# Kernel optimization log

Hardware: AMD Instinct MI355X
Metric: run time of the kernel (lower is better)

## Reference

```python
import jax, jax.numpy as jnp
import numpy as np
import math

SLIDING_WINDOW = 1024  # matches init kwarg

def setup_inputs() -> dict:
    key = jax.random.key(0)
    ks = jax.random.split(key, 6)
    B, S, Hq, Hkv, D = 1, 2048, 32, 8, 128
    NUM_PAGES, STRIDE = 300, 16
    q = jax.random.normal(ks[0], (B, S, Hq, D), dtype=jnp.float32)
    k = jax.random.normal(ks[1], (B, S, Hkv, D), dtype=jnp.float32)
    v = jax.random.normal(ks[2], (B, S, Hkv, D), dtype=jnp.float32)
    sink = jax.random.normal(ks[3], (Hq,), dtype=jnp.float32)
    cache_state = jnp.zeros((NUM_PAGES, STRIDE, 2, Hkv, D), dtype=jnp.float32)
    seq_block_ids = jax.random.randint(ks[4], (B, S // STRIDE), 0, NUM_PAGES, dtype=jnp.int64)
    return {"q": q, "k": k, "v": v, "sink": sink,
            "cache_state": cache_state, "seq_block_ids": seq_block_ids}


def reference(q, k, v, sink, cache_state, seq_block_ids):
    B, S, Hq, D = q.shape
    Hkv = k.shape[2]
    stride = cache_state.shape[1]

    # --- paged cache write (prefill side effect) ---
    kv = jnp.stack([k, v], axis=2)                       # [B,S,2,Hkv,D]
    pages = kv.reshape(B * (S // stride), stride, 2, Hkv, D)
    _ = cache_state.at[seq_block_ids.reshape(-1)].set(pages)

    # --- decomposed attention: matmul + mask + softmax(+sink) + matmul ---
    rep = Hq // Hkv
    ke = jnp.repeat(k, rep, axis=2)                      # [B,S,Hq,D] (GQA expand)
    ve = jnp.repeat(v, rep, axis=2)
    scale = 1.0 / math.sqrt(D)
    scores = jnp.einsum('bihd,bjhd->bhij', q, ke) * scale  # [B,Hq,S,S]

    i = jnp.arange(S)[:, None]
    j = jnp.arange(S)[None, :]
    allowed = (j <= i) & (i - j < SLIDING_WINDOW)        # causal + sliding window
    neg = jnp.finfo(scores.dtype).min
    logits = jnp.where(allowed, scores, neg)

    # attention sink: extra per-head logit appended; contributes to denominator only
    sink_l = jnp.broadcast_to(sink[None, :, None, None], (B, Hq, S, 1))
    probs = jax.nn.softmax(jnp.concatenate([logits, sink_l], axis=-1), axis=-1)[..., :S]

    out = jnp.einsum('bhij,bjhd->bihd', probs, ve)       # [B,S,Hq,D]
    return out
```

## Files before the change

kernel.cpp:

```cpp
#include <hip/hip_runtime.h>
#include <hip/hip_bf16.h>


#define S_LEN 2048
#define DH    128
#define HQ    32
#define HKV   8
#define WIN   1024
#define BR    64
#define BC    32
#define NT    (S_LEN / BC)
#define FM    16.0f
#define TILE_CH 512

typedef unsigned short u16;
typedef __attribute__((ext_vector_type(8))) short  short8;
typedef __attribute__((ext_vector_type(4))) float  floatx4;
typedef __attribute__((ext_vector_type(4))) unsigned int uintx4;

__device__ __forceinline__ unsigned rne1(float a) {
    unsigned u = __float_as_uint(a);
    return (u + 0x7FFFu + ((u >> 16) & 1u)) >> 16;
}
__device__ __forceinline__ unsigned rne_pk(float a, float b) {
    return rne1(a) | (rne1(b) << 16);
}

__global__ __launch_bounds__(256) void pack_kv(const float* __restrict__ kg,
                                               const float* __restrict__ vg,
                                               u16* __restrict__ kp,
                                               u16* __restrict__ vtp)
{
    __shared__ float Vs[BC][DH + 1];
    const int b   = blockIdx.x;
    const int hk  = b >> 6;
    const int jt  = b & 63;
    const int tid = threadIdx.x;
    const int j0  = jt * BC;

    #pragma unroll
    for (int t = 0; t < 4; t++) {
        int idx = tid + t * 256;
        int j   = idx >> 5;
        int dc  = idx & 31;
        floatx4 f = *(const floatx4*)(vg + ((size_t)(j0 + j) * HKV + hk) * DH + dc * 4);
        Vs[j][dc * 4 + 0] = f[0]; Vs[j][dc * 4 + 1] = f[1];
        Vs[j][dc * 4 + 2] = f[2]; Vs[j][dc * 4 + 3] = f[3];
    }

    u16* kpt = kp + (size_t)b * TILE_CH * 8;
    #pragma unroll
    for (int t = 0; t < 2; t++) {
        int c = tid + t * 256;
        int row = c >> 4, cc = c & 15;
        const float* p = kg + ((size_t)(j0 + row) * HKV + hk) * DH + cc * 8;
        floatx4 f0 = *(const floatx4*)p;
        floatx4 f1 = *(const floatx4*)(p + 4);
        int pc = (row << 4) | (cc ^ (row & 7));
        *(uintx4*)(kpt + pc * 8) =
            (uintx4){rne_pk(f0[0], f0[1]), rne_pk(f0[2], f0[3]),
                     rne_pk(f1[0], f1[1]), rne_pk(f1[2], f1[3])};
    }
    __syncthreads();

    u16* vpt = vtp + (size_t)b * TILE_CH * 8;
    #pragma unroll
    for (int t = 0; t < 2; t++) {
        int q  = tid + t * 256;
        int dd = q >> 2, c = q & 3;
        unsigned w0 = rne_pk(Vs[c * 4 + 0][dd], Vs[c * 4 + 16][dd]);
        unsigned w1 = rne_pk(Vs[c * 4 + 1][dd], Vs[c * 4 + 17][dd]);
        unsigned w2 = rne_pk(Vs[c * 4 + 2][dd], Vs[c * 4 + 18][dd]);
        unsigned w3 = rne_pk(Vs[c * 4 + 3][dd], Vs[c * 4 + 19][dd]);
        int qp = (dd << 2) | (c ^ ((dd >> 2) & 3));
        *(uintx4*)(vpt + qp * 8) = (uintx4){w0, w1, w2, w3};
    }
}

__launch_bounds__(256, 4)
__global__ void fa_kernel(const float* __restrict__ qg,
                          const u16* __restrict__ kp,
                          const u16* __restrict__ vtp,
                          const float* __restrict__ sg,
                          float* __restrict__ outg)
{
    __shared__ __align__(16) u16 Kt[2][TILE_CH * 8];
    __shared__ __align__(16) u16 Vt[2][TILE_CH * 8];
    __shared__ __align__(16) u16 Pb[BR * 40];

    const int tid  = threadIdx.x;
    const int w    = tid >> 6;
    const int lane = tid & 63;
    const int quad = lane >> 4;
    const int l16  = lane & 15;

    const int qb = blockIdx.x / HQ;
    const int h  = blockIdx.x % HQ;
    const int hk = h >> 2;
    const int i0 = qb * BR;
    const int m0 = i0 + w * 16;

    short8 qf[4];
    {
        const float* qrow = qg + ((size_t)(m0 + l16) * HQ + h) * DH;
        #pragma unroll
        for (int kk = 0; kk < 4; kk++) {
            const float* p = qrow + kk * 32 + quad * 8;
            floatx4 f0 = *(const floatx4*)p;
            floatx4 f1 = *(const floatx4*)(p + 4);
            uintx4 u = (uintx4){rne_pk(f0[0], f0[1]), rne_pk(f0[2], f0[3]),
                                rne_pk(f1[0], f1[1]), rne_pk(f1[2], f1[3])};
            qf[kk] = *(short8*)&u;
        }
    }

    floatx4 acc[8];
    #pragma unroll
    for (int i = 0; i < 8; i++) acc[i] = (floatx4){0.f, 0.f, 0.f, 0.f};
    float l_part[4] = {0.f, 0.f, 0.f, 0.f};

    int c_r[4];
    #pragma unroll
    for (int r = 0; r < 4; r++) c_r[r] = m0 + quad * 4 + r - l16;

    int jlo = i0 - (WIN - 1); if (jlo < 0) jlo = 0;
    const int jt_lo = jlo >> 5;
    const int jt_hi = (i0 + BR - 1) >> 5;

    const float SC2 = 0.08838834764831845f * 1.4426950408889634f;

    const int ch0 = w * 64 + lane;
    auto stage = [&](int bb, int jt) {
        const u16* kpt = kp  + ((size_t)(hk * NT + jt)) * TILE_CH * 8;
        const u16* vpt = vtp + ((size_t)(hk * NT + jt)) * TILE_CH * 8;
        #pragma unroll
        for (int it = 0; it < 2; it++) {
            int ch = ch0 + it * 256;
            __builtin_amdgcn_global_load_lds(
                (const __attribute__((address_space(1))) unsigned*)(kpt + ch * 8),
                (__attribute__((address_space(3))) unsigned*)(&Kt[bb][ch * 8]), 16, 0, 0);
            __builtin_amdgcn_global_load_lds(
                (const __attribute__((address_space(1))) unsigned*)(vpt + ch * 8),
                (__attribute__((address_space(3))) unsigned*)(&Vt[bb][ch * 8]), 16, 0, 0);
        }
    };

    stage(0, jt_lo);
    int bb = 0;

    for (int jt = jt_lo; jt <= jt_hi; jt++) {
        const int j0 = jt << 5;

        __syncthreads();

        if (jt < jt_hi) stage(bb ^ 1, jt + 1);

        floatx4 sc[2];
        sc[0] = (floatx4){0.f, 0.f, 0.f, 0.f};
        sc[1] = (floatx4){0.f, 0.f, 0.f, 0.f};
        #pragma unroll
        for (int kk = 0; kk < 4; kk++) {
            #pragma unroll
            for (int n = 0; n < 2; n++) {
                int row = n * 16 + l16;
                int cc  = kk * 4 + quad;
                int pc  = (row << 4) | (cc ^ (row & 7));
                short8 kf = *(const short8*)(&Kt[bb][pc * 8]);
                sc[n] = __builtin_amdgcn_mfma_f32_16x16x32_bf16(qf[kk], kf, sc[n], 0, 0, 0);
            }
        }

        const int prow0 = w * 16 + quad * 4;
        const bool interior = (j0 + (BC - 1) <= i0) && (j0 >= i0 + BR - WIN);
        if (interior) {
            #pragma unroll
            for (int r = 0; r < 4; r++) {
                float p0 = exp2f(fmaf(sc[0][r], SC2, -FM));
                float p1 = exp2f(fmaf(sc[1][r], SC2, -FM));
                l_part[r] += p0 + p1;
                *(unsigned*)(&Pb[(prow0 + r) * 40 + l16 * 2]) = rne_pk(p0, p1);
            }
        } else {
            #pragma unroll
            for (int r = 0; r < 4; r++) {
                bool a0 = (j0 <= c_r[r]) && (j0 > c_r[r] - WIN);
                bool a1 = (j0 + 16 <= c_r[r]) && (j0 + 16 > c_r[r] - WIN);
                float p0 = a0 ? exp2f(fmaf(sc[0][r], SC2, -FM)) : 0.f;
                float p1 = a1 ? exp2f(fmaf(sc[1][r], SC2, -FM)) : 0.f;
                l_part[r] += p0 + p1;
                *(unsigned*)(&Pb[(prow0 + r) * 40 + l16 * 2]) = rne_pk(p0, p1);
            }
        }

        {
            short8 pf = *(const short8*)(&Pb[(w * 16 + l16) * 40 + quad * 8]);
            #pragma unroll
            for (int nf = 0; nf < 8; nf++) {
                int dd = nf * 16 + l16;
                int qp = (dd << 2) | (quad ^ ((dd >> 2) & 3));
                short8 vf = *(const short8*)(&Vt[bb][qp * 8]);
                acc[nf] = __builtin_amdgcn_mfma_f32_16x16x32_bf16(pf, vf, acc[nf], 0, 0, 0);
            }
        }
        bb ^= 1;
    }

    const float sk2 = exp2f(fmaf(sg[h], 1.4426950408889634f, -FM));
    float inv[4];
    #pragma unroll
    for (int r = 0; r < 4; r++) {
        float l = l_part[r];
        #pragma unroll
        for (int off = 1; off < 16; off <<= 1)
            l += __shfl_xor(l, off);
        inv[r] = 1.f / (l + sk2);
    }
    #pragma unroll
    for (int nf = 0; nf < 8; nf++) {
        int d = nf * 16 + l16;
        #pragma unroll
        for (int r = 0; r < 4; r++) {
            int ig = m0 + quad * 4 + r;
            outg[((size_t)ig * HQ + h) * DH + d] = acc[nf][r] * inv[r];
        }
    }
}

__launch_bounds__(256, 4)
__global__ void fa_fallback(const float* __restrict__ qg,
                            const float* __restrict__ kg,
                            const float* __restrict__ vg,
                            const float* __restrict__ sg,
                            float* __restrict__ outg)
{
    __shared__ __align__(16) u16 Kt[BC * DH];
    __shared__ __align__(16) u16 Vt[DH * BC];
    __shared__ __align__(16) u16 Pb[BR * 40];

    const int tid  = threadIdx.x;
    const int w    = tid >> 6;
    const int lane = tid & 63;
    const int quad = lane >> 4;
    const int l16  = lane & 15;

    const int qb = blockIdx.x / HQ;
    const int h  = blockIdx.x % HQ;
    const int hk = h >> 2;
    const int i0 = qb * BR;
    const int m0 = i0 + w * 16;

    short8 qf[4];
    {
        const float* qrow = qg + ((size_t)(m0 + l16) * HQ + h) * DH;
        #pragma unroll
        for (int kk = 0; kk < 4; kk++) {
            const float* p = qrow + kk * 32 + quad * 8;
            floatx4 f0 = *(const floatx4*)p;
            floatx4 f1 = *(const floatx4*)(p + 4);
            uintx4 u = (uintx4){rne_pk(f0[0], f0[1]), rne_pk(f0[2], f0[3]),
                                rne_pk(f1[0], f1[1]), rne_pk(f1[2], f1[3])};
            qf[kk] = *(short8*)&u;
        }
    }

    floatx4 acc[8];
    #pragma unroll
    for (int i = 0; i < 8; i++) acc[i] = (floatx4){0.f, 0.f, 0.f, 0.f};
    float l_part[4] = {0.f, 0.f, 0.f, 0.f};

    int jlo = i0 - (WIN - 1); if (jlo < 0) jlo = 0;
    const int jt_lo = jlo >> 5;
    const int jt_hi = (i0 + BR - 1) >> 5;
    const float SC2 = 0.08838834764831845f * 1.4426950408889634f;

    for (int jt = jt_lo; jt <= jt_hi; jt++) {
        const int j0 = jt << 5;
        __syncthreads();
        #pragma unroll
        for (int it = 0; it < 2; it++) {
            int g   = tid + 256 * it;
            int row = g >> 4, cc = g & 15;
            int pc  = (row << 4) | (cc ^ (row & 7));
            const float* kpp = kg + ((size_t)(j0 + row) * HKV + hk) * DH + cc * 8;
            floatx4 f0 = *(const floatx4*)kpp;
            floatx4 f1 = *(const floatx4*)(kpp + 4);
            *(uintx4*)(&Kt[pc * 8]) =
                (uintx4){rne_pk(f0[0], f0[1]), rne_pk(f0[2], f0[3]),
                         rne_pk(f1[0], f1[1]), rne_pk(f1[2], f1[3])};
        }
        #pragma unroll
        for (int it = 0; it < 2; it++) {
            int g  = tid + 256 * it;
            int d  = g & 127, jc = g >> 7;
            const float* vp = vg + ((size_t)(j0 + jc * 8) * HKV + hk) * DH + d;
            float e0 = vp[0 * HKV * DH], e1 = vp[1 * HKV * DH];
            float e2 = vp[2 * HKV * DH], e3 = vp[3 * HKV * DH];
            float e4 = vp[4 * HKV * DH], e5 = vp[5 * HKV * DH];
            float e6 = vp[6 * HKV * DH], e7 = vp[7 * HKV * DH];
            int pc = (d << 2) | (jc ^ ((d >> 2) & 3));
            *(uintx4*)(&Vt[pc * 8]) =
                (uintx4){rne_pk(e0, e1), rne_pk(e2, e3), rne_pk(e4, e5), rne_pk(e6, e7)};
        }
        __syncthreads();

        floatx4 sc[2];
        sc[0] = (floatx4){0.f, 0.f, 0.f, 0.f};
        sc[1] = (floatx4){0.f, 0.f, 0.f, 0.f};
        #pragma unroll
        for (int kk = 0; kk < 4; kk++) {
            #pragma unroll
            for (int n = 0; n < 2; n++) {
                int row = n * 16 + l16;
                int cc  = kk * 4 + quad;
                int pc  = (row << 4) | (cc ^ (row & 7));
                short8 kf = *(const short8*)(&Kt[pc * 8]);
                sc[n] = __builtin_amdgcn_mfma_f32_16x16x32_bf16(qf[kk], kf, sc[n], 0, 0, 0);
            }
        }
        #pragma unroll
        for (int r = 0; r < 4; r++) {
            int   i_g = m0 + quad * 4 + r;
            int   jg0 = j0 + l16, jg1 = j0 + 16 + l16;
            bool  a0  = (jg0 <= i_g) && (i_g - jg0 < WIN);
            bool  a1  = (jg1 <= i_g) && (i_g - jg1 < WIN);
            float p0  = a0 ? exp2f(fmaf(sc[0][r], SC2, -FM)) : 0.f;
            float p1  = a1 ? exp2f(fmaf(sc[1][r], SC2, -FM)) : 0.f;
            l_part[r] += p0 + p1;
            int prow = w * 16 + quad * 4 + r;
            Pb[prow * 40 + 2 * l16]     = (u16)rne1(p0);
            Pb[prow * 40 + 2 * l16 + 1] = (u16)rne1(p1);
        }
        {
            short8 pf = *(const short8*)(&Pb[(w * 16 + l16) * 40 + quad * 8]);
            #pragma unroll
            for (int nf = 0; nf < 8; nf++) {
                int dd = nf * 16 + l16;
                int qp = (dd << 2) | (quad ^ ((dd >> 2) & 3));
                short8 vf = *(const short8*)(&Vt[qp * 8]);
                acc[nf] = __builtin_amdgcn_mfma_f32_16x16x32_bf16(pf, vf, acc[nf], 0, 0, 0);
            }
        }
    }

    const float sk2 = exp2f(fmaf(sg[h], 1.4426950408889634f, -FM));
    float inv[4];
    #pragma unroll
    for (int r = 0; r < 4; r++) {
        float l = l_part[r];
        #pragma unroll
        for (int off = 1; off < 16; off <<= 1)
            l += __shfl_xor(l, off);
        inv[r] = 1.f / (l + sk2);
    }
    #pragma unroll
    for (int nf = 0; nf < 8; nf++) {
        int d = nf * 16 + l16;
        #pragma unroll
        for (int r = 0; r < 4; r++) {
            int ig = m0 + quad * 4 + r;
            outg[((size_t)ig * HQ + h) * DH + d] = acc[nf][r] * inv[r];
        }
    }
}

extern "C" void kernel_launch(void* const* d_in, const int* in_sizes, int n_in,
                              void* d_out, int out_size, void* d_ws, size_t ws_size,
                              hipStream_t stream) {
    const float* q  = (const float*)d_in[0];
    const float* k  = (const float*)d_in[1];
    const float* v  = (const float*)d_in[2];
    const float* sk = (const float*)d_in[3];
    float* out = (float*)d_out;

    const size_t tile_elems = (size_t)HKV * NT * TILE_CH * 8;
    const size_t need = 2 * tile_elems * sizeof(u16);

    if (ws_size >= need) {
        u16* kp  = (u16*)d_ws;
        u16* vtp = kp + tile_elems;
        pack_kv<<<dim3(HKV * NT), 256, 0, stream>>>(k, v, kp, vtp);
        fa_kernel<<<dim3((S_LEN / BR) * HQ), 256, 0, stream>>>(q, kp, vtp, sk, out);
    } else {
        fa_fallback<<<dim3((S_LEN / BR) * HQ), 256, 0, stream>>>(q, k, v, sk, out);
    }
}
```

Baseline: 168.5 us.

## Use 2 waves per block with 32 rows each and reorder blocks for balance

The attention kernel now runs 128 threads (2 waves) per block, and each wave computes two 16-row groups. Every K and V fragment read from LDS therefore feeds two MFMAs, which halves LDS fragment traffic per FLOP but doubles accumulator registers. The block index is remapped so that query tiles of light and heavy cost (the causal/window triangle) are interleaved, which balances load across the dispatch. The fallback path's P store is also changed to a single packed 32-bit write.

```diff
diff --git a/kernel.cpp b/kernel.cpp
--- a/kernel.cpp
+++ b/kernel.cpp
@@ -77,7 +77,7 @@
     }
 }
 
-__launch_bounds__(256, 4)
+__launch_bounds__(128, 2)
 __global__ void fa_kernel(const float* __restrict__ qg,
                           const u16* __restrict__ kp,
                           const u16* __restrict__ vtp,
@@ -94,15 +94,21 @@
     const int quad = lane >> 4;
     const int l16  = lane & 15;
 
-    const int qb = blockIdx.x / HQ;
-    const int h  = blockIdx.x % HQ;
+    const int bid = blockIdx.x;
+    const int t4  = bid >> 8;
+    const int h   = (bid & 255) >> 3;
+    const int u3  = bid & 7;
+    const int qbt[4] = {u3, 15 - u3, 16 + u3, 31 - u3};
+    const int qb  = qbt[t4];
+
     const int hk = h >> 2;
     const int i0 = qb * BR;
-    const int m0 = i0 + w * 16;
-
-    short8 qf[4];
-    {
-        const float* qrow = qg + ((size_t)(m0 + l16) * HQ + h) * DH;
+    const int m0 = i0 + w * 32;
+
+    short8 qf[2][4];
+    #pragma unroll
+    for (int rh = 0; rh < 2; rh++) {
+        const float* qrow = qg + ((size_t)(m0 + rh * 16 + l16) * HQ + h) * DH;
         #pragma unroll
         for (int kk = 0; kk < 4; kk++) {
             const float* p = qrow + kk * 32 + quad * 8;
@@ -110,18 +116,16 @@
             floatx4 f1 = *(const floatx4*)(p + 4);
             uintx4 u = (uintx4){rne_pk(f0[0], f0[1]), rne_pk(f0[2], f0[3]),
                                 rne_pk(f1[0], f1[1]), rne_pk(f1[2], f1[3])};
-            qf[kk] = *(short8*)&u;
-        }
-    }
-
-    floatx4 acc[8];
-    #pragma unroll
-    for (int i = 0; i < 8; i++) acc[i] = (floatx4){0.f, 0.f, 0.f, 0.f};
-    float l_part[4] = {0.f, 0.f, 0.f, 0.f};
-
-    int c_r[4];
-    #pragma unroll
-    for (int r = 0; r < 4; r++) c_r[r] = m0 + quad * 4 + r - l16;
+            qf[rh][kk] = *(short8*)&u;
+        }
+    }
+
+    floatx4 acc[2][8];
+    #pragma unroll
+    for (int rh = 0; rh < 2; rh++)
+        #pragma unroll
+        for (int i = 0; i < 8; i++) acc[rh][i] = (floatx4){0.f, 0.f, 0.f, 0.f};
+    float l_part[2][4] = {{0.f,0.f,0.f,0.f},{0.f,0.f,0.f,0.f}};
 
     int jlo = i0 - (WIN - 1); if (jlo < 0) jlo = 0;
     const int jt_lo = jlo >> 5;
@@ -129,13 +133,12 @@
 
     const float SC2 = 0.08838834764831845f * 1.4426950408889634f;
 
-    const int ch0 = w * 64 + lane;
     auto stage = [&](int bb, int jt) {
         const u16* kpt = kp  + ((size_t)(hk * NT + jt)) * TILE_CH * 8;
         const u16* vpt = vtp + ((size_t)(hk * NT + jt)) * TILE_CH * 8;
         #pragma unroll
-        for (int it = 0; it < 2; it++) {
-            int ch = ch0 + it * 256;
+        for (int it = 0; it < 4; it++) {
+            int ch = tid + it * 128;
             __builtin_amdgcn_global_load_lds(
                 (const __attribute__((address_space(1))) unsigned*)(kpt + ch * 8),
                 (__attribute__((address_space(3))) unsigned*)(&Kt[bb][ch * 8]), 16, 0, 0);
@@ -155,73 +158,92 @@
 
         if (jt < jt_hi) stage(bb ^ 1, jt + 1);
 
-        floatx4 sc[2];
-        sc[0] = (floatx4){0.f, 0.f, 0.f, 0.f};
-        sc[1] = (floatx4){0.f, 0.f, 0.f, 0.f};
+        floatx4 sc[2][2];
+        #pragma unroll
+        for (int rh = 0; rh < 2; rh++) {
+            sc[rh][0] = (floatx4){0.f, 0.f, 0.f, 0.f};
+            sc[rh][1] = (floatx4){0.f, 0.f, 0.f, 0.f};
+        }
         #pragma unroll
         for (int kk = 0; kk < 4; kk++) {
             #pragma unroll
-            for (int n = 0; n < 2; n++) {
-                int row = n * 16 + l16;
+            for (int cn = 0; cn < 2; cn++) {
+                int row = cn * 16 + l16;
                 int cc  = kk * 4 + quad;
                 int pc  = (row << 4) | (cc ^ (row & 7));
                 short8 kf = *(const short8*)(&Kt[bb][pc * 8]);
-                sc[n] = __builtin_amdgcn_mfma_f32_16x16x32_bf16(qf[kk], kf, sc[n], 0, 0, 0);
-            }
-        }
-
-        const int prow0 = w * 16 + quad * 4;
+                #pragma unroll
+                for (int rh = 0; rh < 2; rh++)
+                    sc[rh][cn] = __builtin_amdgcn_mfma_f32_16x16x32_bf16(
+                        qf[rh][kk], kf, sc[rh][cn], 0, 0, 0);
+            }
+        }
+
         const bool interior = (j0 + (BC - 1) <= i0) && (j0 >= i0 + BR - WIN);
-        if (interior) {
-            #pragma unroll
-            for (int r = 0; r < 4; r++) {
-                float p0 = exp2f(fmaf(sc[0][r], SC2, -FM));
-                float p1 = exp2f(fmaf(sc[1][r], SC2, -FM));
-                l_part[r] += p0 + p1;
-                *(unsigned*)(&Pb[(prow0 + r) * 40 + l16 * 2]) = rne_pk(p0, p1);
-            }
-        } else {
-            #pragma unroll
-            for (int r = 0; r < 4; r++) {
-                bool a0 = (j0 <= c_r[r]) && (j0 > c_r[r] - WIN);
-                bool a1 = (j0 + 16 <= c_r[r]) && (j0 + 16 > c_r[r] - WIN);
-                float p0 = a0 ? exp2f(fmaf(sc[0][r], SC2, -FM)) : 0.f;
-                float p1 = a1 ? exp2f(fmaf(sc[1][r], SC2, -FM)) : 0.f;
-                l_part[r] += p0 + p1;
-                *(unsigned*)(&Pb[(prow0 + r) * 40 + l16 * 2]) = rne_pk(p0, p1);
+        #pragma unroll
+        for (int rh = 0; rh < 2; rh++) {
+            const int prow0 = w * 32 + rh * 16 + quad * 4;
+            if (interior) {
+                #pragma unroll
+                for (int r = 0; r < 4; r++) {
+                    float p0 = exp2f(fmaf(sc[rh][0][r], SC2, -FM));
+                    float p1 = exp2f(fmaf(sc[rh][1][r], SC2, -FM));
+                    l_part[rh][r] += p0 + p1;
+                    *(unsigned*)(&Pb[(prow0 + r) * 40 + l16 * 2]) = rne_pk(p0, p1);
+                }
+            } else {
+                #pragma unroll
+                for (int r = 0; r < 4; r++) {
+                    int  i_g = m0 + rh * 16 + quad * 4 + r;
+                    bool a0 = (j0 + l16 <= i_g) && (i_g - (j0 + l16) < WIN);
+                    bool a1 = (j0 + 16 + l16 <= i_g) && (i_g - (j0 + 16 + l16) < WIN);
+                    float p0 = a0 ? exp2f(fmaf(sc[rh][0][r], SC2, -FM)) : 0.f;
+                    float p1 = a1 ? exp2f(fmaf(sc[rh][1][r], SC2, -FM)) : 0.f;
+                    l_part[rh][r] += p0 + p1;
+                    *(unsigned*)(&Pb[(prow0 + r) * 40 + l16 * 2]) = rne_pk(p0, p1);
+                }
             }
         }
 
         {
-            short8 pf = *(const short8*)(&Pb[(w * 16 + l16) * 40 + quad * 8]);
+            short8 pf[2];
+            #pragma unroll
+            for (int rh = 0; rh < 2; rh++)
+                pf[rh] = *(const short8*)(&Pb[(w * 32 + rh * 16 + l16) * 40 + quad * 8]);
             #pragma unroll
             for (int nf = 0; nf < 8; nf++) {
                 int dd = nf * 16 + l16;
                 int qp = (dd << 2) | (quad ^ ((dd >> 2) & 3));
                 short8 vf = *(const short8*)(&Vt[bb][qp * 8]);
-                acc[nf] = __builtin_amdgcn_mfma_f32_16x16x32_bf16(pf, vf, acc[nf], 0, 0, 0);
+                #pragma unroll
+                for (int rh = 0; rh < 2; rh++)
+                    acc[rh][nf] = __builtin_amdgcn_mfma_f32_16x16x32_bf16(
+                        pf[rh], vf, acc[rh][nf], 0, 0, 0);
             }
         }
         bb ^= 1;
     }
 
     const float sk2 = exp2f(fmaf(sg[h], 1.4426950408889634f, -FM));
-    float inv[4];
-    #pragma unroll
-    for (int r = 0; r < 4; r++) {
-        float l = l_part[r];
-        #pragma unroll
-        for (int off = 1; off < 16; off <<= 1)
-            l += __shfl_xor(l, off);
-        inv[r] = 1.f / (l + sk2);
-    }
-    #pragma unroll
-    for (int nf = 0; nf < 8; nf++) {
-        int d = nf * 16 + l16;
+    #pragma unroll
+    for (int rh = 0; rh < 2; rh++) {
+        float inv[4];
         #pragma unroll
         for (int r = 0; r < 4; r++) {
-            int ig = m0 + quad * 4 + r;
-            outg[((size_t)ig * HQ + h) * DH + d] = acc[nf][r] * inv[r];
+            float l = l_part[rh][r];
+            #pragma unroll
+            for (int off = 1; off < 16; off <<= 1)
+                l += __shfl_xor(l, off);
+            inv[r] = 1.f / (l + sk2);
+        }
+        #pragma unroll
+        for (int nf = 0; nf < 8; nf++) {
+            int d = nf * 16 + l16;
+            #pragma unroll
+            for (int r = 0; r < 4; r++) {
+                int ig = m0 + rh * 16 + quad * 4 + r;
+                outg[((size_t)ig * HQ + h) * DH + d] = acc[rh][nf][r] * inv[r];
+            }
         }
     }
 }
@@ -327,8 +349,7 @@
             float p1  = a1 ? exp2f(fmaf(sc[1][r], SC2, -FM)) : 0.f;
             l_part[r] += p0 + p1;
             int prow = w * 16 + quad * 4 + r;
-            Pb[prow * 40 + 2 * l16]     = (u16)rne1(p0);
-            Pb[prow * 40 + 2 * l16 + 1] = (u16)rne1(p1);
+            *(unsigned*)(&Pb[prow * 40 + 2 * l16]) = rne_pk(p0, p1);
         }
         {
             short8 pf = *(const short8*)(&Pb[(w * 16 + l16) * 40 + quad * 8]);
@@ -379,7 +400,7 @@
         u16* kp  = (u16*)d_ws;
         u16* vtp = kp + tile_elems;
         pack_kv<<<dim3(HKV * NT), 256, 0, stream>>>(k, v, kp, vtp);
-        fa_kernel<<<dim3((S_LEN / BR) * HQ), 256, 0, stream>>>(q, kp, vtp, sk, out);
+        fa_kernel<<<dim3((S_LEN / BR) * HQ), 128, 0, stream>>>(q, kp, vtp, sk, out);
     } else {
         fa_fallback<<<dim3((S_LEN / BR) * HQ), 256, 0, stream>>>(q, k, v, sk, out);
     }
```

After: 173.6 us. 1.03x slower.
